# Performance work log

Hardware: AMD Instinct MI355X
Metric: run time of the kernel (lower is better)

The kernel has to match this reference:

```python
import jax, jax.numpy as jnp
import numpy as np
import math

ROPE_THETA = 10000.0

def apply_rope(t, pos, theta):
    # t: [b, h, s, d_k] with d_k even; pos: [b, s] int
    d_k = t.shape[-1]
    inv_freq = theta ** (-jnp.arange(0, d_k, 2, dtype=jnp.float32) / d_k)  # [d_k/2]
    angles = pos.astype(jnp.float32)[..., None] * inv_freq  # [b, s, d_k/2]
    cos = jnp.cos(angles)[:, None, :, :]  # [b, 1, s, d_k/2]
    sin = jnp.sin(angles)[:, None, :, :]
    t_even = t[..., 0::2]
    t_odd = t[..., 1::2]
    out_even = cos * t_even - sin * t_odd
    out_odd = sin * t_even + cos * t_odd
    # interleave back: [..., d_k/2, 2] -> [..., d_k]
    return jnp.stack([out_even, out_odd], axis=-1).reshape(t.shape)

def setup_inputs() -> dict:
    key = jax.random.key(0)
    k1, k2, k3, k4, k5 = jax.random.split(key, 5)
    b, s, d_model = 2, 2048, 1024
    std = math.sqrt(2.0 / (2 * d_model))
    return {
        "x": jax.random.normal(k1, (b, s, d_model), dtype=jnp.float32),
        "token_positions": jnp.broadcast_to(jnp.arange(s, dtype=jnp.int32), (b, s)),
        "W_Q": jax.random.normal(k2, (d_model, d_model), dtype=jnp.float32) * std,
        "W_K": jax.random.normal(k3, (d_model, d_model), dtype=jnp.float32) * std,
        "W_V": jax.random.normal(k4, (d_model, d_model), dtype=jnp.float32) * std,
        "W_O": jax.random.normal(k5, (d_model, d_model), dtype=jnp.float32) * std,
    }

def reference(x, token_positions, W_Q, W_K, W_V, W_O):
    b, s, d_model = x.shape
    n_heads = 16
    d_k = d_model // n_heads

    def proj(W):
        # x @ W^T then split heads: [b, s, d_model] -> [b, h, s, d_k]
        y = jnp.einsum('bsd,ed->bse', x, W)
        return y.reshape(b, s, n_heads, d_k).transpose(0, 2, 1, 3)

    Q = apply_rope(proj(W_Q), token_positions, ROPE_THETA)
    K = apply_rope(proj(W_K), token_positions, ROPE_THETA)
    V = proj(W_V)

    scores = jnp.einsum('bhqd,bhkd->bhqk', Q, K) / math.sqrt(d_k)
    causal = jnp.tril(jnp.ones((s, s), dtype=bool))  # True = keep
    scores = jnp.where(causal, scores, -jnp.inf)
    attn = jax.nn.softmax(scores, axis=-1)
    out = jnp.einsum('bhqk,bhkd->bhqd', attn, V)
    out = out.transpose(0, 2, 1, 3).reshape(b, s, d_model)  # merge heads
    return jnp.einsum('bse,de->bsd', out, W_O)
```

## Files before the change

kernel.cpp:

```cpp
#include <hip/hip_runtime.h>
#include <hip/hip_bf16.h>

typedef __attribute__((ext_vector_type(8))) short short8;
typedef __attribute__((ext_vector_type(4))) short short4v;
typedef __attribute__((ext_vector_type(4))) float f32x4;

#define LN10000_DIV32 0.2878231366242558f
#define SCALE_Q_LOG2E 0.18033688011112042f
#define EXP_BIAS 12.0f

__device__ __forceinline__ unsigned short f2bf(float f){
  union { float fv; unsigned u; } a; a.fv = f;
  return (unsigned short)((a.u + 0x7fffu + ((a.u >> 16) & 1u)) >> 16);
}

__global__ __launch_bounds__(256) void convert_all(
    const float* __restrict__ x, const float* __restrict__ wq,
    const float* __restrict__ wk, const float* __restrict__ wv,
    const float* __restrict__ wo, unsigned short* __restrict__ dst,
    float2* __restrict__ tab)
{
  size_t t = (size_t)blockIdx.x * 256 + threadIdx.x;
  if (t < 65536UL){
    const int s = (int)(t >> 5), ip = (int)(t & 31);
    float invf = __expf(-(float)ip * LN10000_DIV32);
    float ang = (float)s * invf;
    tab[t] = make_float2(__cosf(ang), __sinf(ang));
  }
  size_t e = t * 8;
  const float* src; size_t off;
  if (e < 4194304UL)      { src = x;  off = e; }
  else if (e < 5242880UL) { src = wq; off = e - 4194304UL; }
  else if (e < 6291456UL) { src = wk; off = e - 5242880UL; }
  else if (e < 7340032UL) { src = wv; off = e - 6291456UL; }
  else                    { src = wo; off = e - 7340032UL; }
  float4 f0 = *(const float4*)(src + off);
  float4 f1 = *(const float4*)(src + off + 4);
  short8 o;
  o[0] = (short)f2bf(f0.x); o[1] = (short)f2bf(f0.y);
  o[2] = (short)f2bf(f0.z); o[3] = (short)f2bf(f0.w);
  o[4] = (short)f2bf(f1.x); o[5] = (short)f2bf(f1.y);
  o[6] = (short)f2bf(f1.z); o[7] = (short)f2bf(f1.w);
  *(short8*)(dst + e) = o;
}

__global__ __launch_bounds__(512, 1) void gemm_qkv(
    const unsigned short* __restrict__ Xb, const unsigned short* __restrict__ Wb,
    const int* __restrict__ positions, const float2* __restrict__ tab,
    unsigned short* __restrict__ Qb, unsigned short* __restrict__ Kb,
    unsigned short* __restrict__ Vtb)
{
  __shared__ __align__(16) unsigned short As[3*8192];
  __shared__ __align__(16) unsigned short Bs[3*6144];
  f32x4 acc[4][6] = {};
  const int tid = threadIdx.x, lane = tid & 63, w = tid >> 6;
  const int wm = w >> 1, wn = w & 1;
  const int fr = lane & 15, fq = lane >> 4;
  const int id  = blockIdx.x;
  const int xcd = id & 7;
  const int lid = id >> 3;
  const int m0 = (lid & 15) * 256;
  const int n0 = (xcd*2 + (lid >> 4)) * 192;
  const int ph = ((fq ^ ((fr + (fr >> 2)) & 3))) * 8;
  const bool isA = (w < 4);
  const int t255 = tid & 255;

#define STAGEQ(kt, buf) do {                                                        \
    if (isA){                                                                       \
      _Pragma("unroll")                                                             \
      for (int i_ = 0; i_ < 4; ++i_){                                               \
        const int c_ = i_*256 + t255;                    \
        const int row_ = c_ >> 2, cd_ = c_ & 3;                                     \
        const int sc_ = ((cd_ ^ ((row_ + (row_ >> 2)) & 3))) << 3;                  \
        const unsigned short* ga_ = Xb + (size_t)(m0 + row_) * 1024 + (kt)*32 + sc_;\
        __builtin_amdgcn_global_load_lds((const __attribute__((address_space(1))) void*)ga_, \
            (__attribute__((address_space(3))) void*)(As + (buf)*8192 + c_*8), 16, 0, 0);    \
      }                                                                             \
    } else {                                                                        \
      _Pragma("unroll")                                                             \
      for (int i_ = 0; i_ < 3; ++i_){                                               \
        const int c_ = i_*256 + t255;                     \
        const int row_ = c_ >> 2, cd_ = c_ & 3;                                     \
        const int sc_ = ((cd_ ^ ((row_ + (row_ >> 2)) & 3))) << 3;                  \
        const unsigned short* gb_ = Wb + (size_t)(n0 + row_) * 1024 + (kt)*32 + sc_;\
        __builtin_amdgcn_global_load_lds((const __attribute__((address_space(1))) void*)gb_, \
            (__attribute__((address_space(3))) void*)(Bs + (buf)*6144 + c_*8), 16, 0, 0);    \
      }                                                                             \
    }                                                                               \
  } while(0)

  STAGEQ(0, 0);
  STAGEQ(1, 1);
  for (int t = 0; t < 32; ++t){
    const int cur = t % 3;
    if (t + 2 < 32) STAGEQ(t + 2, (t + 2) % 3);
    if (t < 30){
      if (isA) asm volatile("s_waitcnt vmcnt(8)" ::: "memory");
      else     asm volatile("s_waitcnt vmcnt(6)" ::: "memory");
    } else if (t == 30){
      if (isA) asm volatile("s_waitcnt vmcnt(4)" ::: "memory");
      else     asm volatile("s_waitcnt vmcnt(3)" ::: "memory");
    } else {
      asm volatile("s_waitcnt vmcnt(0)" ::: "memory");
    }
    __builtin_amdgcn_s_barrier();
    asm volatile("" ::: "memory");
    const unsigned short* as = As + cur*8192;
    const unsigned short* bs = Bs + cur*6144;
    short8 af[4], bfv[6];
    #pragma unroll
    for (int mf = 0; mf < 4; ++mf)
      af[mf] = *(const short8*)(as + (wm*64 + mf*16 + fr) * 32 + ph);
    #pragma unroll
    for (int nf = 0; nf < 6; ++nf)
      bfv[nf] = *(const short8*)(bs + (wn*96 + nf*16 + fr) * 32 + ph);
    __builtin_amdgcn_s_setprio(1);
    #pragma unroll
    for (int mf = 0; mf < 4; ++mf)
      #pragma unroll
      for (int nf = 0; nf < 6; ++nf)
        acc[mf][nf] = __builtin_amdgcn_mfma_f32_16x16x32_bf16(af[mf], bfv[nf], acc[mf][nf], 0, 0, 0);
    __builtin_amdgcn_s_setprio(0);
    asm volatile("" ::: "memory");
    __builtin_amdgcn_s_barrier();
  }
#undef STAGEQ

  #pragma unroll
  for (int mf = 0; mf < 4; ++mf){
    int pm[4];
    #pragma unroll
    for (int r = 0; r < 4; ++r){
      const int m = m0 + wm*64 + mf*16 + fq*4 + r;
      pm[r] = positions[m] & 2047;
    }
    const int mbase = m0 + wm*64 + mf*16 + fq*4;
    const int b = mbase >> 11;
    const int s0 = mbase & 2047;
    #pragma unroll
    for (int nf = 0; nf < 6; ++nf){
      const int n = n0 + wn*96 + nf*16 + fr;
      const int seg = n >> 10;
      const int h = (n & 1023) >> 6, d = n & 63;
      const size_t bh = (size_t)b * 16 + h;
      if (seg == 2){
        short4v pack;
        #pragma unroll
        for (int r = 0; r < 4; ++r)
          pack[r] = (short)f2bf(acc[mf][nf][r]);
        *(short4v*)&Vtb[(bh*64 + d)*2048 + s0] = pack;
      } else {
        const int ip = d >> 1;
        #pragma unroll
        for (int r = 0; r < 4; ++r){
          float v = acc[mf][nf][r];
          float pv = __shfl_xor(v, 1);
          const float2 cs = tab[(pm[r] << 5) + ip];
          float outv = (d & 1) ? (cs.x * v + cs.y * pv)
                               : (cs.x * v - cs.y * pv);
          if (seg == 0) outv *= SCALE_Q_LOG2E;
          const unsigned short ob = f2bf(outv);
          const int s = s0 + r;
          if (seg == 0) Qb[(bh*2048 + s)*64 + d] = ob;
          else          Kb[(bh*2048 + s)*64 + d] = ob;
        }
      }
    }
  }
}

__global__ __launch_bounds__(256) void attn_kernel(
    const unsigned short* __restrict__ Qb, const unsigned short* __restrict__ Kb,
    const unsigned short* __restrict__ Vtb, unsigned short* __restrict__ Ob)
{
  __shared__ __align__(16) unsigned short Ks[2][4096];
  __shared__ __align__(16) unsigned short Vs[2][4096];
  __shared__ __align__(16) unsigned short Plds[4][16][64];

  const int tid = threadIdx.x, lane = tid & 63, w = tid >> 6;
  const int fr = lane & 15, fq = lane >> 4;

  const int i = blockIdx.x;
  const int bh = (i & 7) | (((i >> 3) & 3) << 3);
  const int tile = 31 - (i >> 5);
  const int b = bh >> 4, h = bh & 15;
  const int q0 = tile * 64 + w * 16;
  const size_t qk_base = (size_t)bh * 2048 * 64;
  const unsigned short* kbase = Kb + qk_base;
  const unsigned short* vbase = Vtb + (size_t)bh * 64 * 2048;

  const unsigned short* qp = Qb + qk_base + (size_t)(q0 + fr) * 64 + fq * 8;
  short8 aq0 = *(const short8*)qp;
  short8 aq1 = *(const short8*)(qp + 32);

  f32x4 accO[4] = {};
  float lrun = 0.f;
  const int qrow = q0 + fr;
  const int nt = tile + 1;
  const int sw3 = (fr & 7) << 2;

#define STAGE_KV(t_, buf_) do {                                                     \
    const int kv0_ = (t_) * 64;                                                     \
    _Pragma("unroll")                                                               \
    for (int ii_ = 0; ii_ < 2; ++ii_){                                              \
      const int chunk_ = ii_ * 256 + tid;                                           \
      const int row_ = chunk_ >> 3, cd_ = chunk_ & 7;                               \
      const int sc_ = (cd_ ^ (row_ & 7)) << 3;                                      \
      const unsigned short* ksrc_ = kbase + (size_t)(kv0_ + row_) * 64 + sc_;       \
      const unsigned short* vsrc_ = vbase + (size_t)row_ * 2048 + kv0_ + sc_;       \
      __builtin_amdgcn_global_load_lds((const __attribute__((address_space(1))) void*)ksrc_, \
          (__attribute__((address_space(3))) void*)(&Ks[buf_][0] + chunk_*8), 16, 0, 0);     \
      __builtin_amdgcn_global_load_lds((const __attribute__((address_space(1))) void*)vsrc_, \
          (__attribute__((address_space(3))) void*)(&Vs[buf_][0] + chunk_*8), 16, 0, 0);     \
    }                                                                               \
  } while(0)

  STAGE_KV(0, 0);
  for (int t = 0; t < nt; ++t){
    const int cur = t & 1;
    const int kv0 = t * 64;
    if (t + 1 < nt){
      STAGE_KV(t + 1, cur ^ 1);
      asm volatile("s_waitcnt vmcnt(4)" ::: "memory");
    } else {
      asm volatile("s_waitcnt vmcnt(0)" ::: "memory");
    }
    __builtin_amdgcn_s_barrier();
    asm volatile("" ::: "memory");
    const unsigned short* ks = &Ks[cur][0];
    const unsigned short* vs = &Vs[cur][0];

    f32x4 sT[4];
    #pragma unroll
    for (int kf = 0; kf < 4; ++kf){
      const int row = kf*16 + fr;
      const int swr = row & 7;
      short8 k0 = *(const short8*)(ks + row*64 + ((fq ^ swr) << 3));
      short8 k1 = *(const short8*)(ks + row*64 + (((4 + fq) ^ swr) << 3));
      f32x4 s = {0.f, 0.f, 0.f, 0.f};
      s = __builtin_amdgcn_mfma_f32_16x16x32_bf16(k0, aq0, s, 0, 0, 0);
      s = __builtin_amdgcn_mfma_f32_16x16x32_bf16(k1, aq1, s, 0, 0, 0);
      sT[kf] = s;
    }
    if (t == nt - 1){
      #pragma unroll
      for (int kf = 0; kf < 4; ++kf)
        #pragma unroll
        for (int r = 0; r < 4; ++r){
          const int kvcol = kv0 + kf*16 + fq*4 + r;
          if (kvcol > qrow) sT[kf][r] = -1e30f;
        }
    }
    float p[4][4];
    float rs = 0.f;
    #pragma unroll
    for (int kf = 0; kf < 4; ++kf)
      #pragma unroll
      for (int r = 0; r < 4; ++r){
        p[kf][r] = __builtin_amdgcn_exp2f(sT[kf][r] - EXP_BIAS);
        rs += p[kf][r];
      }
    rs += __shfl_xor(rs, 16);
    rs += __shfl_xor(rs, 32);
    lrun += rs;
    unsigned* prow = (unsigned*)&Plds[w][fr][0];
    #pragma unroll
    for (int kf = 0; kf < 4; ++kf)
      #pragma unroll
      for (int jj = 0; jj < 2; ++jj){
        unsigned pk;
        asm("v_cvt_pk_bf16_f32 %0, %1, %2" : "=v"(pk) : "v"(p[kf][2*jj]), "v"(p[kf][2*jj+1]));
        prow[(kf*8 + fq*2 + jj) ^ sw3] = pk;
      }
    asm volatile("s_waitcnt lgkmcnt(0)" ::: "memory");
    const unsigned* crow = (const unsigned*)&Plds[w][fr][0];
    short8 ap0 = *(const short8*)&crow[(fq*4) ^ sw3];
    short8 ap1 = *(const short8*)&crow[(16 + fq*4) ^ sw3];
    __builtin_amdgcn_s_setprio(1);
    #pragma unroll
    for (int dblk = 0; dblk < 4; ++dblk){
      const int d = dblk*16 + fr;
      const int swd = d & 7;
      short8 bv0 = *(const short8*)(vs + d*64 + ((fq ^ swd) << 3));
      short8 bv1 = *(const short8*)(vs + d*64 + (((4 + fq) ^ swd) << 3));
      accO[dblk] = __builtin_amdgcn_mfma_f32_16x16x32_bf16(ap0, bv0, accO[dblk], 0, 0, 0);
      accO[dblk] = __builtin_amdgcn_mfma_f32_16x16x32_bf16(ap1, bv1, accO[dblk], 0, 0, 0);
    }
    __builtin_amdgcn_s_setprio(0);
    asm volatile("" ::: "memory");
    __builtin_amdgcn_s_barrier();
  }
#undef STAGE_KV
  float lq[4];
  #pragma unroll
  for (int r = 0; r < 4; ++r)
    lq[r] = __shfl(lrun, fq*4 + r);
  #pragma unroll
  for (int dblk = 0; dblk < 4; ++dblk)
    #pragma unroll
    for (int r = 0; r < 4; ++r){
      const int s = q0 + fq*4 + r;
      const float o = accO[dblk][r] / lq[r];
      Ob[((size_t)b*2048 + s)*1024 + h*64 + dblk*16 + fr] = f2bf(o);
    }
}

__global__ __launch_bounds__(256) void gemm_out(
    const unsigned short* __restrict__ Obf, const unsigned short* __restrict__ Wb,
    float* __restrict__ out)
{
  __shared__ __align__(16) unsigned short As[3*4096];
  __shared__ __align__(16) unsigned short Bs[3*2048];
  f32x4 acc[4][2] = {};
  const int tid = threadIdx.x, lane = tid & 63, w = tid >> 6;
  const int wm = w >> 1, wn = w & 1;
  const int fr = lane & 15, fq = lane >> 4;
  const int id  = blockIdx.x;
  const int xcd = id & 7;
  const int lid = id >> 3;
  const int m0 = (xcd*4 + (lid & 3)) * 128;
  const int n0 = (lid >> 2) * 64;
  const int ph = ((fq ^ ((fr + (fr >> 2)) & 3))) * 8;

#define STAGEO(kt, buf) do {                                                        \
    _Pragma("unroll")                                                               \
    for (int i_ = 0; i_ < 2; ++i_){                                                 \
      const int c_ = i_*256 + tid;                                                  \
      const int row_ = c_ >> 2, cd_ = c_ & 3;                                       \
      const int sc_ = ((cd_ ^ ((row_ + (row_ >> 2)) & 3))) << 3;                    \
      const unsigned short* ga_ = Obf + (size_t)(m0 + row_) * 1024 + (kt)*32 + sc_; \
      __builtin_amdgcn_global_load_lds((const __attribute__((address_space(1))) void*)ga_, \
          (__attribute__((address_space(3))) void*)(As + (buf)*4096 + c_*8), 16, 0, 0);    \
    }                                                                               \
    {                                                                               \
      const int c_ = tid;                                                           \
      const int row_ = c_ >> 2, cd_ = c_ & 3;                                       \
      const int sc_ = ((cd_ ^ ((row_ + (row_ >> 2)) & 3))) << 3;                    \
      const unsigned short* gb_ = Wb + (size_t)(n0 + row_) * 1024 + (kt)*32 + sc_;  \
      __builtin_amdgcn_global_load_lds((const __attribute__((address_space(1))) void*)gb_, \
          (__attribute__((address_space(3))) void*)(Bs + (buf)*2048 + c_*8), 16, 0, 0);    \
    }                                                                               \
  } while(0)

  STAGEO(0, 0);
  STAGEO(1, 1);
  for (int t = 0; t < 32; ++t){
    const int cur = t % 3;
    if (t + 2 < 32) STAGEO(t + 2, (t + 2) % 3);
    if (t < 30)       asm volatile("s_waitcnt vmcnt(6)" ::: "memory");
    else if (t == 30) asm volatile("s_waitcnt vmcnt(3)" ::: "memory");
    else              asm volatile("s_waitcnt vmcnt(0)" ::: "memory");
    __builtin_amdgcn_s_barrier();
    asm volatile("" ::: "memory");
    const unsigned short* as = As + cur*4096;
    const unsigned short* bs = Bs + cur*2048;
    short8 af[4], bfv[2];
    #pragma unroll
    for (int mf = 0; mf < 4; ++mf)
      af[mf] = *(const short8*)(as + (wm*64 + mf*16 + fr) * 32 + ph);
    #pragma unroll
    for (int nf = 0; nf < 2; ++nf)
      bfv[nf] = *(const short8*)(bs + (wn*32 + nf*16 + fr) * 32 + ph);
    #pragma unroll
    for (int mf = 0; mf < 4; ++mf)
      #pragma unroll
      for (int nf = 0; nf < 2; ++nf)
        acc[mf][nf] = __builtin_amdgcn_mfma_f32_16x16x32_bf16(af[mf], bfv[nf], acc[mf][nf], 0, 0, 0);
    asm volatile("" ::: "memory");
    __builtin_amdgcn_s_barrier();
  }
#undef STAGEO

  #pragma unroll
  for (int mf = 0; mf < 4; ++mf)
    #pragma unroll
    for (int nf = 0; nf < 2; ++nf){
      const int n = n0 + wn*32 + nf*16 + fr;
      #pragma unroll
      for (int r = 0; r < 4; ++r){
        const int m = m0 + wm*64 + mf*16 + fq*4 + r;
        out[(size_t)m * 1024 + n] = acc[mf][nf][r];
      }
    }
}

extern "C" void kernel_launch(void* const* d_in, const int* in_sizes, int n_in,
                              void* d_out, int out_size, void* d_ws, size_t ws_size,
                              hipStream_t stream) {
  const float* x  = (const float*)d_in[0];
  const int* pos  = (const int*)d_in[1];
  const float* wq = (const float*)d_in[2];
  const float* wk = (const float*)d_in[3];
  const float* wv = (const float*)d_in[4];
  const float* wo = (const float*)d_in[5];
  float* out = (float*)d_out;

  unsigned short* ws = (unsigned short*)d_ws;
  unsigned short* Xb   = ws;
  unsigned short* Wqkv = ws + 4194304UL;
  unsigned short* Wo   = ws + 7340032UL;
  unsigned short* Qb   = ws + 8388608UL;
  unsigned short* Kb   = ws + 12582912UL;
  unsigned short* Vt   = ws + 16777216UL;
  unsigned short* Ob   = ws + 20971520UL;
  float2* tab          = (float2*)(ws + 25165824UL);

  convert_all<<<4096, 256, 0, stream>>>(x, wq, wk, wv, wo, ws, tab);

  gemm_qkv<<<256, 512, 0, stream>>>(Xb, Wqkv, pos, tab, Qb, Kb, Vt);

  attn_kernel<<<1024, 256, 0, stream>>>(Qb, Kb, Vt, Ob);

  gemm_out<<<512, 256, 0, stream>>>(Ob, Wo, out);
}
```

Measured before the change: 110.7 us.

## Restructure QKV GEMM to BK=64 double buffering with sliced staging

The QKV projection GEMM now uses a K-tile of 64 instead of 32, and replaces the three-stage LDS ring with two larger buffers. Each K-step is split into four MFMA phases. The loads for the next tile are issued in two slices between phases, and the LDS swizzle is changed to an 8-chunk XOR pattern. The aim is to halve the number of loop iterations and their barriers and to overlap global-to-LDS copies with compute more evenly. The cost is more LDS per block and shallower prefetch depth, which can expose memory latency.

```diff
diff --git a/kernel.cpp b/kernel.cpp
--- a/kernel.cpp
+++ b/kernel.cpp
@@ -50,8 +50,8 @@
     unsigned short* __restrict__ Qb, unsigned short* __restrict__ Kb,
     unsigned short* __restrict__ Vtb)
 {
-  __shared__ __align__(16) unsigned short As[3*8192];
-  __shared__ __align__(16) unsigned short Bs[3*6144];
+  __shared__ __align__(16) unsigned short As[2*16384];
+  __shared__ __align__(16) unsigned short Bs[2*12288];
   f32x4 acc[4][6] = {};
   const int tid = threadIdx.x, lane = tid & 63, w = tid >> 6;
   const int wm = w >> 1, wn = w & 1;
@@ -61,70 +61,115 @@
   const int lid = id >> 3;
   const int m0 = (lid & 15) * 256;
   const int n0 = (xcd*2 + (lid >> 4)) * 192;
-  const int ph = ((fq ^ ((fr + (fr >> 2)) & 3))) * 8;
   const bool isA = (w < 4);
   const int t255 = tid & 255;
 
-#define STAGEQ(kt, buf) do {                                                        \
+#define STAGE_SLICE(kt, buf, s_) do {                                               \
     if (isA){                                                                       \
       _Pragma("unroll")                                                             \
       for (int i_ = 0; i_ < 4; ++i_){                                               \
-        const int c_ = i_*256 + t255;                    \
-        const int row_ = c_ >> 2, cd_ = c_ & 3;                                     \
-        const int sc_ = ((cd_ ^ ((row_ + (row_ >> 2)) & 3))) << 3;                  \
-        const unsigned short* ga_ = Xb + (size_t)(m0 + row_) * 1024 + (kt)*32 + sc_;\
+        const int c_ = (s_)*1024 + i_*256 + t255;                      \
+        const int row_ = c_ >> 3, cd_ = c_ & 7;                                     \
+        const int sc_ = (cd_ ^ (row_ & 7)) << 3;                                    \
+        const unsigned short* ga_ = Xb + (size_t)(m0 + row_) * 1024 + (kt)*64 + sc_;\
         __builtin_amdgcn_global_load_lds((const __attribute__((address_space(1))) void*)ga_, \
-            (__attribute__((address_space(3))) void*)(As + (buf)*8192 + c_*8), 16, 0, 0);    \
+            (__attribute__((address_space(3))) void*)(As + (buf)*16384 + c_*8), 16, 0, 0);   \
       }                                                                             \
     } else {                                                                        \
       _Pragma("unroll")                                                             \
       for (int i_ = 0; i_ < 3; ++i_){                                               \
-        const int c_ = i_*256 + t255;                     \
-        const int row_ = c_ >> 2, cd_ = c_ & 3;                                     \
-        const int sc_ = ((cd_ ^ ((row_ + (row_ >> 2)) & 3))) << 3;                  \
-        const unsigned short* gb_ = Wb + (size_t)(n0 + row_) * 1024 + (kt)*32 + sc_;\
+        const int c_ = (s_)*768 + i_*256 + t255;                       \
+        const int row_ = c_ >> 3, cd_ = c_ & 7;                                     \
+        const int sc_ = (cd_ ^ (row_ & 7)) << 3;                                    \
+        const unsigned short* gb_ = Wb + (size_t)(n0 + row_) * 1024 + (kt)*64 + sc_;\
         __builtin_amdgcn_global_load_lds((const __attribute__((address_space(1))) void*)gb_, \
-            (__attribute__((address_space(3))) void*)(Bs + (buf)*6144 + c_*8), 16, 0, 0);    \
+            (__attribute__((address_space(3))) void*)(Bs + (buf)*12288 + c_*8), 16, 0, 0);   \
       }                                                                             \
     }                                                                               \
   } while(0)
 
-  STAGEQ(0, 0);
-  STAGEQ(1, 1);
-  for (int t = 0; t < 32; ++t){
-    const int cur = t % 3;
-    if (t + 2 < 32) STAGEQ(t + 2, (t + 2) % 3);
-    if (t < 30){
+  STAGE_SLICE(0, 0, 0); STAGE_SLICE(0, 0, 1);
+  STAGE_SLICE(1, 1, 0); STAGE_SLICE(1, 1, 1);
+
+  const int row_a0 = wm*64 + fr;
+  const int row_b0 = wn*96 + fr;
+
+  for (int t = 0; t < 16; ++t){
+    const int cur = t & 1;
+    if (t == 0){
       if (isA) asm volatile("s_waitcnt vmcnt(8)" ::: "memory");
       else     asm volatile("s_waitcnt vmcnt(6)" ::: "memory");
-    } else if (t == 30){
-      if (isA) asm volatile("s_waitcnt vmcnt(4)" ::: "memory");
-      else     asm volatile("s_waitcnt vmcnt(3)" ::: "memory");
     } else {
       asm volatile("s_waitcnt vmcnt(0)" ::: "memory");
     }
     __builtin_amdgcn_s_barrier();
     asm volatile("" ::: "memory");
-    const unsigned short* as = As + cur*8192;
-    const unsigned short* bs = Bs + cur*6144;
+    const unsigned short* as = As + cur*16384;
+    const unsigned short* bs = Bs + cur*12288;
     short8 af[4], bfv[6];
-    #pragma unroll
-    for (int mf = 0; mf < 4; ++mf)
-      af[mf] = *(const short8*)(as + (wm*64 + mf*16 + fr) * 32 + ph);
-    #pragma unroll
-    for (int nf = 0; nf < 6; ++nf)
-      bfv[nf] = *(const short8*)(bs + (wn*96 + nf*16 + fr) * 32 + ph);
+
+#define LDA(mf_, kh_) do { \
+      const int row_ = row_a0 + (mf_)*16; \
+      const int c_ = ((kh_)*4 + fq) ^ (row_ & 7); \
+      af[mf_] = *(const short8*)(as + row_*64 + c_*8); } while(0)
+#define LDB(nf_, kh_) do { \
+      const int row_ = row_b0 + (nf_)*16; \
+      const int c_ = ((kh_)*4 + fq) ^ (row_ & 7); \
+      bfv[nf_] = *(const short8*)(bs + row_*64 + c_*8); } while(0)
+
+    if (t >= 1 && t + 1 < 16) STAGE_SLICE(t + 1, cur ^ 1, 0);
+    LDA(0,0); LDA(1,0); LDA(2,0); LDA(3,0);
+    LDB(0,0); LDB(1,0); LDB(2,0);
     __builtin_amdgcn_s_setprio(1);
     #pragma unroll
     for (int mf = 0; mf < 4; ++mf)
       #pragma unroll
-      for (int nf = 0; nf < 6; ++nf)
+      for (int nf = 0; nf < 3; ++nf)
         acc[mf][nf] = __builtin_amdgcn_mfma_f32_16x16x32_bf16(af[mf], bfv[nf], acc[mf][nf], 0, 0, 0);
     __builtin_amdgcn_s_setprio(0);
     asm volatile("" ::: "memory");
     __builtin_amdgcn_s_barrier();
+    asm volatile("" ::: "memory");
+
+    if (t >= 1 && t + 1 < 16) STAGE_SLICE(t + 1, cur ^ 1, 1);
+    LDB(3,0); LDB(4,0); LDB(5,0);
+    __builtin_amdgcn_s_setprio(1);
+    #pragma unroll
+    for (int mf = 0; mf < 4; ++mf)
+      #pragma unroll
+      for (int nf = 3; nf < 6; ++nf)
+        acc[mf][nf] = __builtin_amdgcn_mfma_f32_16x16x32_bf16(af[mf], bfv[nf], acc[mf][nf], 0, 0, 0);
+    __builtin_amdgcn_s_setprio(0);
+    asm volatile("" ::: "memory");
+    __builtin_amdgcn_s_barrier();
+    asm volatile("" ::: "memory");
+
+    LDA(0,1); LDA(1,1); LDA(2,1); LDA(3,1);
+    LDB(3,1); LDB(4,1); LDB(5,1);
+    __builtin_amdgcn_s_setprio(1);
+    #pragma unroll
+    for (int mf = 0; mf < 4; ++mf)
+      #pragma unroll
+      for (int nf = 3; nf < 6; ++nf)
+        acc[mf][nf] = __builtin_amdgcn_mfma_f32_16x16x32_bf16(af[mf], bfv[nf], acc[mf][nf], 0, 0, 0);
+    __builtin_amdgcn_s_setprio(0);
+    asm volatile("" ::: "memory");
+    __builtin_amdgcn_s_barrier();
+    asm volatile("" ::: "memory");
+
+    LDB(0,1); LDB(1,1); LDB(2,1);
+    __builtin_amdgcn_s_setprio(1);
+    #pragma unroll
+    for (int mf = 0; mf < 4; ++mf)
+      #pragma unroll
+      for (int nf = 0; nf < 3; ++nf)
+        acc[mf][nf] = __builtin_amdgcn_mfma_f32_16x16x32_bf16(af[mf], bfv[nf], acc[mf][nf], 0, 0, 0);
+    __builtin_amdgcn_s_setprio(0);
+    asm volatile("" ::: "memory");
+#undef LDA
+#undef LDB
   }
-#undef STAGEQ
+#undef STAGE_SLICE
 
   #pragma unroll
   for (int mf = 0; mf < 4; ++mf){
```

Measured after the change: 104.8 us. -5.3%, faster.
